# Optimization experiments

Hardware: AMD Instinct MI355X
Metric: run time of the kernel (lower is better)

The kernel has to match this reference:

```python
import jax, jax.numpy as jnp
import numpy as np

DIMS = [2048, 1024, 512, 256, 128, 64, 32, 16, 8, 4, 2]
IN_CH = [3, 8, 32, 64, 64, 64, 128, 256, 512, 512, 512]
FEAT = [8, 32, 64, 64, 64, 128, 256, 512, 512, 512, 1024]
B = 512
K = 16


def setup_inputs() -> dict:
    key = jax.random.key(0)
    keys = jax.random.split(key, 64)
    inp = {"x": jax.random.normal(keys[0], (B, 3, 2048), dtype=jnp.float32)}
    for i, d in enumerate(DIMS):
        inp[f"c{i}"] = jax.random.randint(keys[1 + i], (d,), 0, 3, dtype=jnp.int64)
    for i in range(11):
        cin, f = IN_CH[i], FEAT[i]
        inp[f"W{i+1}"] = jax.random.normal(keys[20 + 2 * i], (3 * f, cin), dtype=jnp.float32) / jnp.sqrt(jnp.float32(cin))
        inp[f"b{i+1}"] = jnp.zeros((3 * f,), dtype=jnp.float32)
    inp["Wfc"] = jax.random.normal(keys[60], (K, 1024), dtype=jnp.float32) / jnp.sqrt(jnp.float32(1024))
    inp["bfc"] = jnp.zeros((K,), dtype=jnp.float32)
    return inp


def _kdconv(x, W, b, sel, featdim, dim):
    # pointwise conv (kernel size 1) + relu: [B, in, dim] -> [B, 3*featdim, dim]
    y = jax.nn.relu(jnp.einsum('oi,bid->bod', W, x) + b[None, :, None])
    bsz = y.shape[0]
    # faithful to torch: view [B, featdim, 3*dim], then gather index d*3 + sel[d]
    y = y.reshape(bsz, featdim, 3 * dim)
    idx = sel + 3 * jnp.arange(dim, dtype=sel.dtype)
    y = jnp.take(y, idx, axis=2)                       # [B, featdim, dim]
    y = y.reshape(bsz, featdim, dim // 2, 2)
    return jnp.max(y, axis=-1)                          # [B, featdim, dim//2]


def reference(x, c0, c1, c2, c3, c4, c5, c6, c7, c8, c9, c10,
              W1, b1, W2, b2, W3, b3, W4, b4, W5, b5, W6, b6,
              W7, b7, W8, b8, W9, b9, W10, b10, W11, b11, Wfc, bfc):
    cs = [c0, c1, c2, c3, c4, c5, c6, c7, c8, c9, c10]
    Ws = [W1, W2, W3, W4, W5, W6, W7, W8, W9, W10, W11]
    bs = [b1, b2, b3, b4, b5, b6, b7, b8, b9, b10, b11]
    y = x
    for i in range(11):
        y = _kdconv(y, Ws[i], bs[i], cs[i], FEAT[i], DIMS[i])
    y = y.reshape(-1, 1024)
    logits = y @ Wfc.T + bfc
    return jax.nn.log_softmax(logits, axis=1)
```

## Files before the change

kernel.cpp:

```cpp
#include <hip/hip_runtime.h>
#include <cstdint>
#include <cmath>


typedef __attribute__((ext_vector_type(8))) short bhalf8;
typedef __attribute__((ext_vector_type(4))) float floatx4;

__device__ __forceinline__ unsigned short f2bf(float f) {
    uint32_t u = __float_as_uint(f);
    u += 0x7FFFu + ((u >> 16) & 1u);
    return (unsigned short)(u >> 16);
}
__device__ __forceinline__ float bf2f(unsigned short u) {
    return __uint_as_float(((uint32_t)u) << 16);
}

struct WPrep {
    const float* src[5];
    unsigned short* dst[5];
    int n4[5];
};

__global__ __launch_bounds__(256)
void wprep25_kernel(WPrep wp) {
    const int stride = gridDim.x * 256;
    const int g0 = blockIdx.x * 256 + threadIdx.x;
    #pragma unroll
    for (int l = 0; l < 4; ++l) {
        const float4* s = reinterpret_cast<const float4*>(wp.src[l]);
        uint2* d = reinterpret_cast<uint2*>(wp.dst[l]);
        for (int i = g0; i < wp.n4[l]; i += stride) {
            const float4 v = s[i];
            uint2 o;
            o.x = (uint32_t)f2bf(v.x) | ((uint32_t)f2bf(v.y) << 16);
            o.y = (uint32_t)f2bf(v.z) | ((uint32_t)f2bf(v.w) << 16);
            d[i] = o;
        }
    }
}


template<int RB>
__device__ __forceinline__ int swaddr(int row, int colbyte) {
    constexpr int SM = (RB / 16 >= 8) ? 7 : (RB / 16 - 1);
    return row * RB + (colbyte ^ ((row & SM) << 4));
}

template<int CIN>
__device__ __forceinline__ int wswz(int i) {
    constexpr int GPR = CIN / 8;
    constexpr int RB  = CIN * 2;
    const int row = i / GPR, c = i - row * GPR;
    return swaddr<RB>(row, c * 16);
}

template<int DIM, int CIN, int FEAT>
__device__ __forceinline__ void kdlayer(char* pool, int offIn, int offOut,
                                        int qpOff, int offW,
                                        const float* __restrict__ bg, int tid) {
    constexpr int NH  = CIN / 32;
    constexpr int MT  = DIM / 16;
    constexpr int NT  = FEAT / 16;
    constexpr int RBW = CIN * 2;
    constexpr int RBO = FEAT * 2;
    constexpr int WM  = (MT < 8) ? MT : 8;
    constexpr int WN  = 8 / WM;
    constexpr int MPW = MT / WM;
    constexpr int NPW = NT / WN;

    const unsigned short* qp = (const unsigned short*)(pool + qpOff);
    const int wv = tid >> 6, ln = tid & 63;
    const int g = ln >> 4, l15 = ln & 15;
    const int wm = wv % WM, wn = wv / WM;

    bhalf8 aC[MPW][NH];
    uint32_t qpk[MPW];
    #pragma unroll
    for (int i = 0; i < MPW; ++i) {
        const int mt = wm + i * WM;
        const int pa = qp[mt * 16 + l15] & 0xFFF;
        #pragma unroll
        for (int ks = 0; ks < NH; ++ks)
            aC[i][ks] = *(const bhalf8*)(pool + offIn +
                          swaddr<RBW>(pa, (ks * 32 + g * 8) * 2));
        const ushort4 qq = *(const ushort4*)(qp + mt * 16 + g * 4);
        qpk[i] = (uint32_t)(qq.x >> 12) | ((uint32_t)(qq.y >> 12) << 4)
               | ((uint32_t)(qq.z >> 12) << 8) | ((uint32_t)(qq.w >> 12) << 12);
    }

    #pragma unroll
    for (int ntj = 0; ntj < NPW; ++ntj) {
        const int nt = wn * NPW + ntj;
        const int f = nt * 16 + l15;
        bhalf8 bF[3][NH];
        #pragma unroll
        for (int q = 0; q < 3; ++q)
            #pragma unroll
            for (int ks = 0; ks < NH; ++ks)
                bF[q][ks] = *(const bhalf8*)(pool + offW +
                              swaddr<RBW>(3 * f + q, (ks * 32 + g * 8) * 2));
        const float bv0 = bg[3 * f + 0];
        const float bv1 = bg[3 * f + 1];
        const float bv2 = bg[3 * f + 2];
        #pragma unroll
        for (int i = 0; i < MPW; ++i) {
            floatx4 a0 = (floatx4){0.f,0.f,0.f,0.f};
            floatx4 a1 = (floatx4){0.f,0.f,0.f,0.f};
            floatx4 a2 = (floatx4){0.f,0.f,0.f,0.f};
            #pragma unroll
            for (int ks = 0; ks < NH; ++ks) {
                a0 = __builtin_amdgcn_mfma_f32_16x16x32_bf16(aC[i][ks], bF[0][ks], a0, 0, 0, 0);
                a1 = __builtin_amdgcn_mfma_f32_16x16x32_bf16(aC[i][ks], bF[1][ks], a1, 0, 0, 0);
                a2 = __builtin_amdgcn_mfma_f32_16x16x32_bf16(aC[i][ks], bF[2][ks], a2, 0, 0, 0);
            }
            const int mt = wm + i * WM;
            const int j0 = mt * 8 + g * 2;
            float v[4];
            #pragma unroll
            for (int r = 0; r < 4; ++r) {
                const int qi = (qpk[i] >> (4 * r)) & 0xF;
                const float pre = (qi == 0) ? a0[r] : (qi == 1 ? a1[r] : a2[r]);
                const float bq  = (qi == 0) ? bv0  : (qi == 1 ? bv1  : bv2);
                v[r] = pre + bq;
            }
            *(unsigned short*)(pool + offOut + swaddr<RBO>(j0,     f * 2)) =
                f2bf(fmaxf(fmaxf(v[0], v[1]), 0.f));
            *(unsigned short*)(pool + offOut + swaddr<RBO>(j0 + 1, f * 2)) =
                f2bf(fmaxf(fmaxf(v[2], v[3]), 0.f));
        }
    }
}

__global__ __launch_bounds__(512, 4)
void chain_kernel(const float* __restrict__ x,
                  const float* __restrict__ W0, const float* __restrict__ b0f,
                  const int* __restrict__ sel0,
                  const float* __restrict__ W1, const float* __restrict__ b1f,
                  const int* __restrict__ sel1,
                  unsigned short* __restrict__ outp,
                  const unsigned short* __restrict__ w2, const float* __restrict__ b2, const int* __restrict__ s2,
                  const unsigned short* __restrict__ w3, const float* __restrict__ b3, const int* __restrict__ s3,
                  const unsigned short* __restrict__ w4, const float* __restrict__ b4, const int* __restrict__ s4,
                  const unsigned short* __restrict__ w5, const float* __restrict__ b5, const int* __restrict__ s5,
                  WPrep wp, int nrows) {
    const int tid = threadIdx.x;

    if ((int)blockIdx.x >= nrows) {
        const int stride = (gridDim.x - nrows) * 512;
        const int g0 = (blockIdx.x - nrows) * 512 + tid;
        #pragma unroll
        for (int l = 0; l < 5; ++l) {
            const float4* s = reinterpret_cast<const float4*>(wp.src[l]);
            uint2* d = reinterpret_cast<uint2*>(wp.dst[l]);
            for (int i = g0; i < wp.n4[l]; i += stride) {
                const float4 v = s[i];
                uint2 o;
                o.x = (uint32_t)f2bf(v.x) | ((uint32_t)f2bf(v.y) << 16);
                o.y = (uint32_t)f2bf(v.z) | ((uint32_t)f2bf(v.w) << 16);
                d[i] = o;
            }
        }
        return;
    }

    __shared__ __align__(16) char pool[79872];
    const int b = blockIdx.x;

    bhalf8 w3r[3];
    #pragma unroll
    for (int u = 0; u < 3; ++u)
        w3r[u] = ((const bhalf8*)w3)[u * 512 + tid];
    bhalf8 w2r[2];
    w2r[0] = ((const bhalf8*)w2)[tid];
    if (tid < 256) w2r[1] = ((const bhalf8*)w2)[512 + tid];

    float* W0s = (float*)(pool + 47104);
    float* b0s = W0s + 72;
    float* W1s = b0s + 24;
    float* b1s = W1s + 768;
    if (tid < 24) {
        W0s[tid * 3 + 0] = W0[tid * 3 + 0];
        W0s[tid * 3 + 1] = W0[tid * 3 + 1];
        W0s[tid * 3 + 2] = W0[tid * 3 + 2];
        b0s[tid] = b0f[tid];
    }
    if (tid < 96) {
        #pragma unroll
        for (int k = 0; k < 8; ++k) W1s[tid * 8 + k] = W1[tid * 8 + k];
        b1s[tid] = b1f[tid];
    }
    {
        unsigned short* qp2 = (unsigned short*)(pool + 0);
        unsigned short* qp3 = (unsigned short*)(pool + 1024);
        unsigned short* qp4 = (unsigned short*)(pool + 1536);
        unsigned short* qp5 = (unsigned short*)(pool + 1792);
        { const int d = tid;
          const int e = 3 * d + s2[d];
          const int q = (e >= 512) + (e >= 1024);
          qp2[d] = (unsigned short)((q << 12) | (e - q * 512)); }
        if (tid < 256) { const int d = tid;
          const int e = 3 * d + s3[d];
          const int q = (e >= 256) + (e >= 512);
          qp3[d] = (unsigned short)((q << 12) | (e - q * 256)); }
        if (tid < 128) { const int d = tid;
          const int e = 3 * d + s4[d];
          const int q = (e >= 128) + (e >= 256);
          qp4[d] = (unsigned short)((q << 12) | (e - q * 128)); }
        if (tid < 64)  { const int d = tid;
          const int e = 3 * d + s5[d];
          const int q = (e >= 64) + (e >= 128);
          qp5[d] = (unsigned short)((q << 12) | (e - q * 64)); }
    }
    __syncthreads();

    {
        const int j1 = tid;
        const float* xb = x + (size_t)b * 3 * 2048;

        float cols[2][8];
        int q1v[2];
        #pragma unroll
        for (int pos1 = 0; pos1 < 2; ++pos1) {
            const int d1 = 2 * j1 + pos1;
            const int e1 = 3 * d1 + sel1[d1];
            const int q1 = (e1 >= 1024) + (e1 >= 2048);
            const int p1 = e1 - q1 * 1024;
            q1v[pos1] = q1;

            float xv[2][3]; int qq0[2];
            #pragma unroll
            for (int pos0 = 0; pos0 < 2; ++pos0) {
                const int d0 = 2 * p1 + pos0;
                const int e0 = 3 * d0 + sel0[d0];
                const int q0 = (e0 >= 2048) + (e0 >= 4096);
                const int p0 = e0 - q0 * 2048;
                qq0[pos0] = q0;
                xv[pos0][0] = xb[p0];
                xv[pos0][1] = xb[2048 + p0];
                xv[pos0][2] = xb[4096 + p0];
            }
            #pragma unroll
            for (int f = 0; f < 8; ++f) {
                const int r0 = 3 * f + qq0[0], r1 = 3 * f + qq0[1];
                const float v0 = b0s[r0] + W0s[r0*3+0]*xv[0][0] + W0s[r0*3+1]*xv[0][1] + W0s[r0*3+2]*xv[0][2];
                const float v1 = b0s[r1] + W0s[r1*3+0]*xv[1][0] + W0s[r1*3+1]*xv[1][1] + W0s[r1*3+2]*xv[1][2];
                cols[pos1][f] = fmaxf(fmaxf(v0, v1), 0.f);
            }
        }
        #pragma unroll
        for (int gi = 0; gi < 4; ++gi) {
            bhalf8 og;
            #pragma unroll
            for (int fk = 0; fk < 8; ++fk) {
                const int f = gi * 8 + fk;
                const int r0 = 3 * f + q1v[0], r1 = 3 * f + q1v[1];
                float v0 = b1s[r0], v1 = b1s[r1];
                #pragma unroll
                for (int k = 0; k < 8; ++k) {
                    v0 = fmaf(cols[0][k], W1s[r0*8+k], v0);
                    v1 = fmaf(cols[1][k], W1s[r1*8+k], v1);
                }
                og[fk] = (short)f2bf(fmaxf(fmaxf(v0, v1), 0.f));
            }
            *(bhalf8*)(pool + 2048 + swaddr<64>(j1, gi * 16)) = og;
        }
    }
    *(bhalf8*)(pool + 34816 + wswz<32>(tid)) = w2r[0];
    if (tid < 256)
        *(bhalf8*)(pool + 34816 + wswz<32>(512 + tid)) = w2r[1];
    __syncthreads();

    kdlayer<512, 32, 64>(pool, 2048, 47104, 0, 34816, b2, tid);
    __syncthreads();

    bhalf8 w4r[3];
    #pragma unroll
    for (int u = 0; u < 3; ++u)
        w4r[u] = ((const bhalf8*)w4)[u * 512 + tid];
    #pragma unroll
    for (int u = 0; u < 3; ++u)
        *(bhalf8*)(pool + 2048 + wswz<64>(u * 512 + tid)) = w3r[u];
    __syncthreads();

    kdlayer<256, 64, 64>(pool, 47104, 26624, 1024, 2048, b3, tid);
    __syncthreads();

    bhalf8 w5r[6];
    #pragma unroll
    for (int u = 0; u < 6; ++u)
        w5r[u] = ((const bhalf8*)w5)[u * 512 + tid];
    #pragma unroll
    for (int u = 0; u < 3; ++u)
        *(bhalf8*)(pool + 47104 + wswz<64>(u * 512 + tid)) = w4r[u];
    __syncthreads();

    kdlayer<128, 64, 64>(pool, 26624, 71680, 1536, 47104, b4, tid);
    __syncthreads();

    #pragma unroll
    for (int u = 0; u < 6; ++u)
        *(bhalf8*)(pool + 2048 + wswz<64>(u * 512 + tid)) = w5r[u];
    __syncthreads();

    kdlayer<64, 64, 128>(pool, 71680, 51200, 1792, 2048, b5, tid);
    __syncthreads();

    {
        char* dst = (char*)(outp + (size_t)b * 32 * 128);
        const int off = tid * 16;
        const bhalf8 v = *(const bhalf8*)(pool + 51200 +
                                          swaddr<256>(off >> 8, off & 255));
        *(bhalf8*)(dst + off) = v;
    }
}

template<int CIN, int BT>
__global__ __launch_bounds__(256)
void kdmfma_kernel(const unsigned short* __restrict__ act,
                   const unsigned short* __restrict__ Wq,
                   const float* __restrict__ bias,
                   const int*   __restrict__ sel,
                   unsigned short* __restrict__ out,
                   int feat, int dim, int nbt) {
    constexpr int KS  = (CIN >= 128) ? 128 : CIN;
    constexpr int NH  = KS / 32;
    constexpr int LDK = KS + 8;
    constexpr int TPA = 256 / BT;
    constexpr int EA  = KS / TPA;
    constexpr int NSA = EA / 8;
    constexpr int NSW = KS / 32;
    constexpr int MF  = 2;
    constexpr int NF  = (BT == 64) ? 2 : 1;
    __shared__ __align__(16) unsigned short Ab[BT][LDK];
    __shared__ __align__(16) unsigned short Wb[64][LDK];

    const int dimh = dim >> 1;
    const int bt = blockIdx.x % nbt;
    const int j  = blockIdx.x / nbt;
    const int f0 = blockIdx.y * 64;
    const int b0 = bt * BT;

    const int tid  = threadIdx.x;
    const int lane = tid & 63;
    const int wave = tid >> 6;

    const int srowA = tid / TPA;
    const int kgA   = (tid % TPA) * EA;
    const int srowW = tid >> 2;
    const int kgW   = (tid & 3) * (KS / 4);

    const int rowBase = (BT == 64) ? (wave & 1) * 32 : 0;
    const int colBase = (BT == 64) ? (wave >> 1) * 32 : wave * 16;

    floatx4 acc[2][MF][NF];
    #pragma unroll
    for (int pp = 0; pp < 2; ++pp)
        #pragma unroll
        for (int mi = 0; mi < MF; ++mi)
            #pragma unroll
            for (int ni = 0; ni < NF; ++ni)
                acc[pp][mi][ni] = (floatx4){0.f, 0.f, 0.f, 0.f};
    int qv[2];

    #pragma unroll
    for (int pp = 0; pp < 2; ++pp) {
        const int d = 2 * j + pp;
        const int s = sel[d];
        const int e = 3 * d + s;
        const int q = (e >= dim) + (e >= 2 * dim);
        const int p = e - q * dim;
        qv[pp] = q;

        const unsigned short* Ap = act + ((size_t)(b0 + srowA) * dim + p) * CIN + kgA;
        const unsigned short* Wp = Wq + ((size_t)(3 * (f0 + srowW) + q)) * CIN + kgW;

        bhalf8 pa[NSA], pw[NSW];
        #pragma unroll
        for (int u = 0; u < NSA; ++u)
            pa[u] = *reinterpret_cast<const bhalf8*>(Ap + u * 8);
        #pragma unroll
        for (int u = 0; u < NSW; ++u)
            pw[u] = *reinterpret_cast<const bhalf8*>(Wp + u * 8);

        for (int k0 = 0; k0 < CIN; k0 += KS) {
            __syncthreads();
            #pragma unroll
            for (int u = 0; u < NSA; ++u)
                *reinterpret_cast<bhalf8*>(&Ab[srowA][kgA + u * 8]) = pa[u];
            #pragma unroll
            for (int u = 0; u < NSW; ++u)
                *reinterpret_cast<bhalf8*>(&Wb[srowW][kgW + u * 8]) = pw[u];
            if (k0 + KS < CIN) {
                #pragma unroll
                for (int u = 0; u < NSA; ++u)
                    pa[u] = *reinterpret_cast<const bhalf8*>(Ap + k0 + KS + u * 8);
                #pragma unroll
                for (int u = 0; u < NSW; ++u)
                    pw[u] = *reinterpret_cast<const bhalf8*>(Wp + k0 + KS + u * 8);
            }
            __syncthreads();

            #pragma unroll
            for (int ks = 0; ks < NH; ++ks) {
                const int kk = ks * 32 + (lane >> 4) * 8;
                bhalf8 aF[MF], bF[NF];
                #pragma unroll
                for (int mi = 0; mi < MF; ++mi)
                    aF[mi] = *reinterpret_cast<const bhalf8*>(
                        &Ab[rowBase + mi * 16 + (lane & 15)][kk]);
                #pragma unroll
                for (int ni = 0; ni < NF; ++ni)
                    bF[ni] = *reinterpret_cast<const bhalf8*>(
                        &Wb[colBase + ni * 16 + (lane & 15)][kk]);
                #pragma unroll
                for (int mi = 0; mi < MF; ++mi)
                    #pragma unroll
                    for (int ni = 0; ni < NF; ++ni)
                        acc[pp][mi][ni] = __builtin_amdgcn_mfma_f32_16x16x32_bf16(
                            aF[mi], bF[ni], acc[pp][mi][ni], 0, 0, 0);
            }
        }
    }

    const int orow = (lane >> 4) << 2;
    const int ocol = lane & 15;
    #pragma unroll
    for (int mi = 0; mi < MF; ++mi)
        #pragma unroll
        for (int ni = 0; ni < NF; ++ni) {
            const int fc = f0 + colBase + ni * 16 + ocol;
            const float bv0 = bias[3 * fc + qv[0]];
            const float bv1 = bias[3 * fc + qv[1]];
            #pragma unroll
            for (int i = 0; i < 4; ++i) {
                const int br = b0 + rowBase + mi * 16 + orow + i;
                const float v = fmaxf(fmaxf(acc[0][mi][ni][i] + bv0,
                                            acc[1][mi][ni][i] + bv1), 0.f);
                out[((size_t)br * dimh + j) * feat + fc] = f2bf(v);
            }
        }
}

template<int CIN, int BT>
__global__ __launch_bounds__(256)
void kdmfma2_kernel(const unsigned short* __restrict__ act,
                    const unsigned short* __restrict__ Wq,
                    const float* __restrict__ bias,
                    const int*   __restrict__ sel,
                    unsigned short* __restrict__ out,
                    int feat, int dim, int nbt) {
    constexpr int KS  = 128;
    constexpr int NH  = KS / 32;
    constexpr int LDK = KS + 8;
    constexpr int TPA = 256 / BT;
    constexpr int EA  = KS / TPA;
    constexpr int NSA = EA / 8;
    constexpr int NSW = KS / 32;
    constexpr int MF  = 2;
    __shared__ __align__(16) unsigned short Ab[2][BT][LDK];
    __shared__ __align__(16) unsigned short Wb[2][64][LDK];

    const int dimh = dim >> 1;
    const int bt = blockIdx.x % nbt;
    const int j  = blockIdx.x / nbt;
    const int f0 = blockIdx.y * 64;
    const int b0 = bt * BT;

    const int tid  = threadIdx.x;
    const int lane = tid & 63;
    const int wave = tid >> 6;

    const int srowA = tid / TPA;
    const int kgA   = (tid % TPA) * EA;
    const int srowW = tid >> 2;
    const int kgW   = (tid & 3) * (KS / 4);
    const int colBase = wave * 16;

    int qv[2];
    const unsigned short* Ap[2];
    const unsigned short* Wp[2];
    #pragma unroll
    for (int pp = 0; pp < 2; ++pp) {
        const int d = 2 * j + pp;
        const int e = 3 * d + sel[d];
        const int q = (e >= dim) + (e >= 2 * dim);
        const int p = e - q * dim;
        qv[pp] = q;
        Ap[pp] = act + ((size_t)(b0 + srowA) * dim + p) * CIN + kgA;
        Wp[pp] = Wq + ((size_t)(3 * (f0 + srowW) + q)) * CIN + kgW;
    }

    floatx4 acc[2][MF];
    #pragma unroll
    for (int pp = 0; pp < 2; ++pp)
        #pragma unroll
        for (int mi = 0; mi < MF; ++mi)
            acc[pp][mi] = (floatx4){0.f, 0.f, 0.f, 0.f};

    bhalf8 pa[2][NSA], pw[2][NSW];
    #pragma unroll
    for (int pp = 0; pp < 2; ++pp) {
        #pragma unroll
        for (int u = 0; u < NSA; ++u)
            pa[pp][u] = *reinterpret_cast<const bhalf8*>(Ap[pp] + u * 8);
        #pragma unroll
        for (int u = 0; u < NSW; ++u)
            pw[pp][u] = *reinterpret_cast<const bhalf8*>(Wp[pp] + u * 8);
    }

    for (int k0 = 0; k0 < CIN; k0 += KS) {
        __syncthreads();
        #pragma unroll
        for (int pp = 0; pp < 2; ++pp) {
            #pragma unroll
            for (int u = 0; u < NSA; ++u)
                *reinterpret_cast<bhalf8*>(&Ab[pp][srowA][kgA + u * 8]) = pa[pp][u];
            #pragma unroll
            for (int u = 0; u < NSW; ++u)
                *reinterpret_cast<bhalf8*>(&Wb[pp][srowW][kgW + u * 8]) = pw[pp][u];
        }
        if (k0 + KS < CIN) {
            #pragma unroll
            for (int pp = 0; pp < 2; ++pp) {
                #pragma unroll
                for (int u = 0; u < NSA; ++u)
                    pa[pp][u] = *reinterpret_cast<const bhalf8*>(Ap[pp] + k0 + KS + u * 8);
                #pragma unroll
                for (int u = 0; u < NSW; ++u)
                    pw[pp][u] = *reinterpret_cast<const bhalf8*>(Wp[pp] + k0 + KS + u * 8);
            }
        }
        __syncthreads();

        #pragma unroll
        for (int ks = 0; ks < NH; ++ks) {
            const int kk = ks * 32 + (lane >> 4) * 8;
            bhalf8 aF[2][MF], bF[2];
            #pragma unroll
            for (int pp = 0; pp < 2; ++pp) {
                #pragma unroll
                for (int mi = 0; mi < MF; ++mi)
                    aF[pp][mi] = *reinterpret_cast<const bhalf8*>(
                        &Ab[pp][mi * 16 + (lane & 15)][kk]);
                bF[pp] = *reinterpret_cast<const bhalf8*>(
                        &Wb[pp][colBase + (lane & 15)][kk]);
            }
            #pragma unroll
            for (int pp = 0; pp < 2; ++pp)
                #pragma unroll
                for (int mi = 0; mi < MF; ++mi)
                    acc[pp][mi] = __builtin_amdgcn_mfma_f32_16x16x32_bf16(
                        aF[pp][mi], bF[pp], acc[pp][mi], 0, 0, 0);
        }
    }

    const int orow = (lane >> 4) << 2;
    const int ocol = lane & 15;
    #pragma unroll
    for (int mi = 0; mi < MF; ++mi) {
        const int fc = f0 + colBase + ocol;
        const float bv0 = bias[3 * fc + qv[0]];
        const float bv1 = bias[3 * fc + qv[1]];
        #pragma unroll
        for (int i = 0; i < 4; ++i) {
            const int br = b0 + mi * 16 + orow + i;
            const float v = fmaxf(fmaxf(acc[0][mi][i] + bv0,
                                        acc[1][mi][i] + bv1), 0.f);
            out[((size_t)br * dimh + j) * feat + fc] = f2bf(v);
        }
    }
}

__global__ __launch_bounds__(256)
void fc_lsm_kernel(const unsigned short* __restrict__ y,
                   const float* __restrict__ Wfc,
                   const float* __restrict__ bfc,
                   float* __restrict__ out) {
    const int b   = blockIdx.x;
    const int tid = threadIdx.x;
    __shared__ __align__(16) float ys[1024];
    __shared__ float lg[16];

    {
        const ushort4 v = reinterpret_cast<const ushort4*>(y + (size_t)b * 1024)[tid];
        ys[tid * 4 + 0] = bf2f(v.x);
        ys[tid * 4 + 1] = bf2f(v.y);
        ys[tid * 4 + 2] = bf2f(v.z);
        ys[tid * 4 + 3] = bf2f(v.w);
    }
    __syncthreads();

    const int l = tid >> 4, lane = tid & 15;
    const float4* w4 = reinterpret_cast<const float4*>(Wfc + (size_t)l * 1024);
    const float4* y4 = reinterpret_cast<const float4*>(ys);
    float p = 0.f;
    #pragma unroll
    for (int i = 0; i < 16; ++i) {
        const float4 a = y4[lane + 16 * i];
        const float4 w = w4[lane + 16 * i];
        p += a.x * w.x + a.y * w.y + a.z * w.z + a.w * w.w;
    }
    #pragma unroll
    for (int off = 8; off > 0; off >>= 1) p += __shfl_down(p, off, 16);
    if (lane == 0) lg[l] = p + bfc[l];
    __syncthreads();

    if (tid < 16) {
        float m = -1e30f;
        #pragma unroll
        for (int i = 0; i < 16; ++i) m = fmaxf(m, lg[i]);
        float s = 0.f;
        #pragma unroll
        for (int i = 0; i < 16; ++i) s += expf(lg[i] - m);
        out[b * 16 + tid] = lg[tid] - m - logf(s);
    }
}

extern "C" void kernel_launch(void* const* d_in, const int* in_sizes, int n_in,
                              void* d_out, int out_size, void* d_ws, size_t ws_size,
                              hipStream_t stream) {
    static const int LFEAT[11] = {8, 32, 64, 64, 64, 128, 256, 512, 512, 512, 1024};
    static const int LDIM[11]  = {2048, 1024, 512, 256, 128, 64, 32, 16, 8, 4, 2};
    static const int LCIN[11]  = {3, 8, 32, 64, 64, 64, 128, 256, 512, 512, 512};

    const float* x = (const float*)d_in[0];
    const int B = in_sizes[0] / (3 * 2048);

    const size_t slot = (size_t)B * 32 * 512;
    float* bufA = (float*)d_ws;
    float* bufB = bufA + slot;
    unsigned short* wq = (unsigned short*)(bufB + slot);

    const float* W[11]; const float* bi[11]; const int* sl[11];
    for (int i = 0; i < 11; ++i) {
        W[i]  = (const float*)d_in[12 + 2 * i];
        bi[i] = (const float*)d_in[13 + 2 * i];
        sl[i] = (const int*)d_in[1 + i];
    }

    unsigned short* wqp[11];
    {
        size_t off = 0;
        for (int i = 2; i <= 10; ++i) {
            wqp[i] = wq + off;
            off += (size_t)3 * LFEAT[i] * LCIN[i];
        }
    }

    unsigned short* actA = (unsigned short*)bufA;
    unsigned short* actB = (unsigned short*)bufB;

    {
        WPrep wp;
        for (int i = 2; i <= 5; ++i) {
            wp.src[i - 2] = W[i];
            wp.dst[i - 2] = wqp[i];
            wp.n4[i - 2]  = (3 * LFEAT[i] * LCIN[i]) / 4;
        }
        wp.src[4] = nullptr; wp.dst[4] = nullptr; wp.n4[4] = 0;
        wprep25_kernel<<<64, 256, 0, stream>>>(wp);
    }

    {
        WPrep wp;
        for (int i = 6; i <= 10; ++i) {
            wp.src[i - 6] = W[i];
            wp.dst[i - 6] = wqp[i];
            wp.n4[i - 6]  = (3 * LFEAT[i] * LCIN[i]) / 4;
        }
        chain_kernel<<<B + 256, 512, 0, stream>>>(
            x, W[0], bi[0], sl[0], W[1], bi[1], sl[1], actA,
            wqp[2], bi[2], sl[2], wqp[3], bi[3], sl[3],
            wqp[4], bi[4], sl[4], wqp[5], bi[5], sl[5],
            wp, B);
    }

    const int nbt64 = B / 64;
    const int nbt32 = B / 32;

    {   dim3 g((LDIM[6]/2) * nbt64, LFEAT[6]/64);
        kdmfma_kernel<128, 64><<<g, 256, 0, stream>>>(actA, wqp[6], bi[6], sl[6], actB, LFEAT[6], LDIM[6], nbt64); }
    {   dim3 g((LDIM[7]/2) * nbt64, LFEAT[7]/64);
        kdmfma_kernel<256, 64><<<g, 256, 0, stream>>>(actB, wqp[7], bi[7], sl[7], actA, LFEAT[7], LDIM[7], nbt64); }

    {   dim3 g((LDIM[8]/2) * nbt32, LFEAT[8]/64);
        kdmfma2_kernel<512, 32><<<g, 256, 0, stream>>>(actA, wqp[8], bi[8], sl[8], actB, LFEAT[8], LDIM[8], nbt32); }
    {   dim3 g((LDIM[9]/2) * nbt32, LFEAT[9]/64);
        kdmfma2_kernel<512, 32><<<g, 256, 0, stream>>>(actB, wqp[9], bi[9], sl[9], actA, LFEAT[9], LDIM[9], nbt32); }
    {   dim3 g((LDIM[10]/2) * nbt32, LFEAT[10]/64);
        kdmfma2_kernel<512, 32><<<g, 256, 0, stream>>>(actA, wqp[10], bi[10], sl[10], actB, LFEAT[10], LDIM[10], nbt32); }

    fc_lsm_kernel<<<B, 256, 0, stream>>>(actB, (const float*)d_in[34],
                                         (const float*)d_in[35], (float*)d_out);
}
```

Measured before the change: 82.31 us.

## Fuse layer 2-5 weight conversion into chain kernel and retile late MFMA layers

Drops the separate weight-prep kernel for layers 2-5; the chain kernel now reads fp32 weights and converts them to bf16 in registers before writing to shared memory. It also stages x and the layer-0 gather indices in LDS instead of reading them scattered from global memory. Layers 6-7 move from the older kdmfma kernel to kdmfma2 with 32-row batch tiles, and layers 9-10 use 16-row tiles to launch more blocks. The first-iteration barrier is skipped. In exchange the chain kernel holds more registers and reads twice the weight bytes, and the small-tile MFMA layers reuse less data per block.

Measured after the change: 86.69 us. 1.05x slower.

```diff
diff --git a/kernel.cpp b/kernel.cpp
--- a/kernel.cpp
+++ b/kernel.cpp
@@ -13,6 +13,14 @@
 }
 __device__ __forceinline__ float bf2f(unsigned short u) {
     return __uint_as_float(((uint32_t)u) << 16);
+}
+__device__ __forceinline__ bhalf8 cvt8(const float4 a, const float4 b) {
+    bhalf8 r;
+    r[0] = (short)f2bf(a.x); r[1] = (short)f2bf(a.y);
+    r[2] = (short)f2bf(a.z); r[3] = (short)f2bf(a.w);
+    r[4] = (short)f2bf(b.x); r[5] = (short)f2bf(b.y);
+    r[6] = (short)f2bf(b.z); r[7] = (short)f2bf(b.w);
+    return r;
 }
 
 struct WPrep {
@@ -20,25 +28,6 @@
     unsigned short* dst[5];
     int n4[5];
 };
-
-__global__ __launch_bounds__(256)
-void wprep25_kernel(WPrep wp) {
-    const int stride = gridDim.x * 256;
-    const int g0 = blockIdx.x * 256 + threadIdx.x;
-    #pragma unroll
-    for (int l = 0; l < 4; ++l) {
-        const float4* s = reinterpret_cast<const float4*>(wp.src[l]);
-        uint2* d = reinterpret_cast<uint2*>(wp.dst[l]);
-        for (int i = g0; i < wp.n4[l]; i += stride) {
-            const float4 v = s[i];
-            uint2 o;
-            o.x = (uint32_t)f2bf(v.x) | ((uint32_t)f2bf(v.y) << 16);
-            o.y = (uint32_t)f2bf(v.z) | ((uint32_t)f2bf(v.w) << 16);
-            d[i] = o;
-        }
-    }
-}
-
 
 template<int RB>
 __device__ __forceinline__ int swaddr(int row, int colbyte) {
@@ -138,10 +127,10 @@
                   const float* __restrict__ W1, const float* __restrict__ b1f,
                   const int* __restrict__ sel1,
                   unsigned short* __restrict__ outp,
-                  const unsigned short* __restrict__ w2, const float* __restrict__ b2, const int* __restrict__ s2,
-                  const unsigned short* __restrict__ w3, const float* __restrict__ b3, const int* __restrict__ s3,
-                  const unsigned short* __restrict__ w4, const float* __restrict__ b4, const int* __restrict__ s4,
-                  const unsigned short* __restrict__ w5, const float* __restrict__ b5, const int* __restrict__ s5,
+                  const float* __restrict__ w2f, const float* __restrict__ b2, const int* __restrict__ s2,
+                  const float* __restrict__ w3f, const float* __restrict__ b3, const int* __restrict__ s3,
+                  const float* __restrict__ w4f, const float* __restrict__ b4, const int* __restrict__ s4,
+                  const float* __restrict__ w5f, const float* __restrict__ b5, const int* __restrict__ s5,
                   WPrep wp, int nrows) {
     const int tid = threadIdx.x;
 
@@ -166,13 +155,21 @@
     __shared__ __align__(16) char pool[79872];
     const int b = blockIdx.x;
 
-    bhalf8 w3r[3];
-    #pragma unroll
-    for (int u = 0; u < 3; ++u)
-        w3r[u] = ((const bhalf8*)w3)[u * 512 + tid];
-    bhalf8 w2r[2];
-    w2r[0] = ((const bhalf8*)w2)[tid];
-    if (tid < 256) w2r[1] = ((const bhalf8*)w2)[512 + tid];
+    const float4* xg = (const float4*)(x + (size_t)b * 6144);
+    const float4 xr0 = xg[tid], xr1 = xg[512 + tid], xr2 = xg[1024 + tid];
+
+    const float4* w2g = (const float4*)w2f;
+    float4 w2a0 = w2g[2 * tid], w2a1 = w2g[2 * tid + 1];
+    float4 w2b0 = {0,0,0,0}, w2b1 = {0,0,0,0};
+    if (tid < 256) { w2b0 = w2g[2 * (512 + tid)]; w2b1 = w2g[2 * (512 + tid) + 1]; }
+
+    const float4* w3g = (const float4*)w3f;
+    float4 w3r[6];
+    #pragma unroll
+    for (int u = 0; u < 3; ++u) {
+        w3r[2 * u]     = w3g[2 * (u * 512 + tid)];
+        w3r[2 * u + 1] = w3g[2 * (u * 512 + tid) + 1];
+    }
 
     float* W0s = (float*)(pool + 47104);
     float* b0s = W0s + 72;
@@ -210,12 +207,25 @@
           const int e = 3 * d + s5[d];
           const int q = (e >= 64) + (e >= 128);
           qp5[d] = (unsigned short)((q << 12) | (e - q * 64)); }
+        unsigned short* qp0 = (unsigned short*)(pool + 75776);
+        #pragma unroll
+        for (int it = 0; it < 4; ++it) {
+            const int d = it * 512 + tid;
+            const int e = 3 * d + sel0[d];
+            const int q = (e >= 2048) + (e >= 4096);
+            qp0[d] = (unsigned short)((q << 12) | (e - q * 2048));
+        }
+    }
+    {
+        float4* xs4 = (float4*)(pool + 51200);
+        xs4[tid] = xr0; xs4[512 + tid] = xr1; xs4[1024 + tid] = xr2;
     }
     __syncthreads();
 
     {
         const int j1 = tid;
-        const float* xb = x + (size_t)b * 3 * 2048;
+        const float* xs = (const float*)(pool + 51200);
+        const unsigned short* qp0 = (const unsigned short*)(pool + 75776);
 
         float cols[2][8];
         int q1v[2];
@@ -230,14 +240,13 @@
             float xv[2][3]; int qq0[2];
             #pragma unroll
             for (int pos0 = 0; pos0 < 2; ++pos0) {
-                const int d0 = 2 * p1 + pos0;
-                const int e0 = 3 * d0 + sel0[d0];
-                const int q0 = (e0 >= 2048) + (e0 >= 4096);
-                const int p0 = e0 - q0 * 2048;
+                const int c0 = qp0[2 * p1 + pos0];
+                const int q0 = c0 >> 12;
+                const int p0 = c0 & 0xFFF;
                 qq0[pos0] = q0;
-                xv[pos0][0] = xb[p0];
-                xv[pos0][1] = xb[2048 + p0];
-                xv[pos0][2] = xb[4096 + p0];
+                xv[pos0][0] = xs[p0];
+                xv[pos0][1] = xs[2048 + p0];
+                xv[pos0][2] = xs[4096 + p0];
             }
             #pragma unroll
             for (int f = 0; f < 8; ++f) {
@@ -265,41 +274,47 @@
             *(bhalf8*)(pool + 2048 + swaddr<64>(j1, gi * 16)) = og;
         }
     }
-    *(bhalf8*)(pool + 34816 + wswz<32>(tid)) = w2r[0];
+    *(bhalf8*)(pool + 34816 + wswz<32>(tid)) = cvt8(w2a0, w2a1);
     if (tid < 256)
-        *(bhalf8*)(pool + 34816 + wswz<32>(512 + tid)) = w2r[1];
+        *(bhalf8*)(pool + 34816 + wswz<32>(512 + tid)) = cvt8(w2b0, w2b1);
     __syncthreads();
 
     kdlayer<512, 32, 64>(pool, 2048, 47104, 0, 34816, b2, tid);
     __syncthreads();
 
-    bhalf8 w4r[3];
+    const float4* w4g = (const float4*)w4f;
+    float4 w4r[6];
+    #pragma unroll
+    for (int u = 0; u < 3; ++u) {
+        w4r[2 * u]     = w4g[2 * (u * 512 + tid)];
+        w4r[2 * u + 1] = w4g[2 * (u * 512 + tid) + 1];
+    }
     #pragma unroll
     for (int u = 0; u < 3; ++u)
-        w4r[u] = ((const bhalf8*)w4)[u * 512 + tid];
+        *(bhalf8*)(pool + 2048 + wswz<64>(u * 512 + tid)) = cvt8(w3r[2*u], w3r[2*u+1]);
+    __syncthreads();
+
+    kdlayer<256, 64, 64>(pool, 47104, 26624, 1024, 2048, b3, tid);
+    __syncthreads();
+
+    const float4* w5g = (const float4*)w5f;
+    float4 w5r[12];
+    #pragma unroll
+    for (int u = 0; u < 6; ++u) {
+        w5r[2 * u]     = w5g[2 * (u * 512 + tid)];
+        w5r[2 * u + 1] = w5g[2 * (u * 512 + tid) + 1];
+    }
     #pragma unroll
     for (int u = 0; u < 3; ++u)
-        *(bhalf8*)(pool + 2048 + wswz<64>(u * 512 + tid)) = w3r[u];
-    __syncthreads();
-
-    kdlayer<256, 64, 64>(pool, 47104, 26624, 1024, 2048, b3, tid);
-    __syncthreads();
-
-    bhalf8 w5r[6];
+        *(bhalf8*)(pool + 47104 + wswz<64>(u * 512 + tid)) = cvt8(w4r[2*u], w4r[2*u+1]);
+    __syncthreads();
+
+    kdlayer<128, 64, 64>(pool, 26624, 71680, 1536, 47104, b4, tid);
+    __syncthreads();
+
     #pragma unroll
     for (int u = 0; u < 6; ++u)
-        w5r[u] = ((const bhalf8*)w5)[u * 512 + tid];
-    #pragma unroll
-    for (int u = 0; u < 3; ++u)
-        *(bhalf8*)(pool + 47104 + wswz<64>(u * 512 + tid)) = w4r[u];
-    __syncthreads();
-
-    kdlayer<128, 64, 64>(pool, 26624, 71680, 1536, 47104, b4, tid);
-    __syncthreads();
-
-    #pragma unroll
-    for (int u = 0; u < 6; ++u)
-        *(bhalf8*)(pool + 2048 + wswz<64>(u * 512 + tid)) = w5r[u];
+        *(bhalf8*)(pool + 2048 + wswz<64>(u * 512 + tid)) = cvt8(w5r[2*u], w5r[2*u+1]);
     __syncthreads();
 
     kdlayer<64, 64, 128>(pool, 71680, 51200, 1792, 2048, b5, tid);
@@ -312,133 +327,6 @@
                                           swaddr<256>(off >> 8, off & 255));
         *(bhalf8*)(dst + off) = v;
     }
-}
-
-template<int CIN, int BT>
-__global__ __launch_bounds__(256)
-void kdmfma_kernel(const unsigned short* __restrict__ act,
-                   const unsigned short* __restrict__ Wq,
-                   const float* __restrict__ bias,
-                   const int*   __restrict__ sel,
-                   unsigned short* __restrict__ out,
-                   int feat, int dim, int nbt) {
-    constexpr int KS  = (CIN >= 128) ? 128 : CIN;
-    constexpr int NH  = KS / 32;
-    constexpr int LDK = KS + 8;
-    constexpr int TPA = 256 / BT;
-    constexpr int EA  = KS / TPA;
-    constexpr int NSA = EA / 8;
-    constexpr int NSW = KS / 32;
-    constexpr int MF  = 2;
-    constexpr int NF  = (BT == 64) ? 2 : 1;
-    __shared__ __align__(16) unsigned short Ab[BT][LDK];
-    __shared__ __align__(16) unsigned short Wb[64][LDK];
-
-    const int dimh = dim >> 1;
-    const int bt = blockIdx.x % nbt;
-    const int j  = blockIdx.x / nbt;
-    const int f0 = blockIdx.y * 64;
-    const int b0 = bt * BT;
-
-    const int tid  = threadIdx.x;
-    const int lane = tid & 63;
-    const int wave = tid >> 6;
-
-    const int srowA = tid / TPA;
-    const int kgA   = (tid % TPA) * EA;
-    const int srowW = tid >> 2;
-    const int kgW   = (tid & 3) * (KS / 4);
-
-    const int rowBase = (BT == 64) ? (wave & 1) * 32 : 0;
-    const int colBase = (BT == 64) ? (wave >> 1) * 32 : wave * 16;
-
-    floatx4 acc[2][MF][NF];
-    #pragma unroll
-    for (int pp = 0; pp < 2; ++pp)
-        #pragma unroll
-        for (int mi = 0; mi < MF; ++mi)
-            #pragma unroll
-            for (int ni = 0; ni < NF; ++ni)
-                acc[pp][mi][ni] = (floatx4){0.f, 0.f, 0.f, 0.f};
-    int qv[2];
-
-    #pragma unroll
-    for (int pp = 0; pp < 2; ++pp) {
-        const int d = 2 * j + pp;
-        const int s = sel[d];
-        const int e = 3 * d + s;
-        const int q = (e >= dim) + (e >= 2 * dim);
-        const int p = e - q * dim;
-        qv[pp] = q;
-
-        const unsigned short* Ap = act + ((size_t)(b0 + srowA) * dim + p) * CIN + kgA;
-        const unsigned short* Wp = Wq + ((size_t)(3 * (f0 + srowW) + q)) * CIN + kgW;
-
-        bhalf8 pa[NSA], pw[NSW];
-        #pragma unroll
-        for (int u = 0; u < NSA; ++u)
-            pa[u] = *reinterpret_cast<const bhalf8*>(Ap + u * 8);
-        #pragma unroll
-        for (int u = 0; u < NSW; ++u)
-            pw[u] = *reinterpret_cast<const bhalf8*>(Wp + u * 8);
-
-        for (int k0 = 0; k0 < CIN; k0 += KS) {
-            __syncthreads();
-            #pragma unroll
-            for (int u = 0; u < NSA; ++u)
-                *reinterpret_cast<bhalf8*>(&Ab[srowA][kgA + u * 8]) = pa[u];
-            #pragma unroll
-            for (int u = 0; u < NSW; ++u)
-                *reinterpret_cast<bhalf8*>(&Wb[srowW][kgW + u * 8]) = pw[u];
-            if (k0 + KS < CIN) {
-                #pragma unroll
-                for (int u = 0; u < NSA; ++u)
-                    pa[u] = *reinterpret_cast<const bhalf8*>(Ap + k0 + KS + u * 8);
-                #pragma unroll
-                for (int u = 0; u < NSW; ++u)
-                    pw[u] = *reinterpret_cast<const bhalf8*>(Wp + k0 + KS + u * 8);
-            }
-            __syncthreads();
-
-            #pragma unroll
-            for (int ks = 0; ks < NH; ++ks) {
-                const int kk = ks * 32 + (lane >> 4) * 8;
-                bhalf8 aF[MF], bF[NF];
-                #pragma unroll
-                for (int mi = 0; mi < MF; ++mi)
-                    aF[mi] = *reinterpret_cast<const bhalf8*>(
-                        &Ab[rowBase + mi * 16 + (lane & 15)][kk]);
-                #pragma unroll
-                for (int ni = 0; ni < NF; ++ni)
-                    bF[ni] = *reinterpret_cast<const bhalf8*>(
-                        &Wb[colBase + ni * 16 + (lane & 15)][kk]);
-                #pragma unroll
-                for (int mi = 0; mi < MF; ++mi)
-                    #pragma unroll
-                    for (int ni = 0; ni < NF; ++ni)
-                        acc[pp][mi][ni] = __builtin_amdgcn_mfma_f32_16x16x32_bf16(
-                            aF[mi], bF[ni], acc[pp][mi][ni], 0, 0, 0);
-            }
-        }
-    }
-
-    const int orow = (lane >> 4) << 2;
-    const int ocol = lane & 15;
-    #pragma unroll
-    for (int mi = 0; mi < MF; ++mi)
-        #pragma unroll
-        for (int ni = 0; ni < NF; ++ni) {
-            const int fc = f0 + colBase + ni * 16 + ocol;
-            const float bv0 = bias[3 * fc + qv[0]];
-            const float bv1 = bias[3 * fc + qv[1]];
-            #pragma unroll
-            for (int i = 0; i < 4; ++i) {
-                const int br = b0 + rowBase + mi * 16 + orow + i;
-                const float v = fmaxf(fmaxf(acc[0][mi][ni][i] + bv0,
-                                            acc[1][mi][ni][i] + bv1), 0.f);
-                out[((size_t)br * dimh + j) * feat + fc] = f2bf(v);
-            }
-        }
 }
 
 template<int CIN, int BT>
@@ -456,7 +344,7 @@
     constexpr int EA  = KS / TPA;
     constexpr int NSA = EA / 8;
     constexpr int NSW = KS / 32;
-    constexpr int MF  = 2;
+    constexpr int MF  = BT / 16;
     __shared__ __align__(16) unsigned short Ab[2][BT][LDK];
     __shared__ __align__(16) unsigned short Wb[2][64][LDK];
 
@@ -509,7 +397,7 @@
     }
 
     for (int k0 = 0; k0 < CIN; k0 += KS) {
-        __syncthreads();
+        if (k0) __syncthreads();
         #pragma unroll
         for (int pp = 0; pp < 2; ++pp) {
             #pragma unroll
@@ -641,7 +529,7 @@
     unsigned short* wqp[11];
     {
         size_t off = 0;
-        for (int i = 2; i <= 10; ++i) {
+        for (int i = 6; i <= 10; ++i) {
             wqp[i] = wq + off;
             off += (size_t)3 * LFEAT[i] * LCIN[i];
         }
@@ -649,17 +537,6 @@
 
     unsigned short* actA = (unsigned short*)bufA;
     unsigned short* actB = (unsigned short*)bufB;
-
-    {
-        WPrep wp;
-        for (int i = 2; i <= 5; ++i) {
-            wp.src[i - 2] = W[i];
-            wp.dst[i - 2] = wqp[i];
-            wp.n4[i - 2]  = (3 * LFEAT[i] * LCIN[i]) / 4;
-        }
-        wp.src[4] = nullptr; wp.dst[4] = nullptr; wp.n4[4] = 0;
-        wprep25_kernel<<<64, 256, 0, stream>>>(wp);
-    }
 
     {
         WPrep wp;
@@ -670,25 +547,25 @@
         }
         chain_kernel<<<B + 256, 512, 0, stream>>>(
             x, W[0], bi[0], sl[0], W[1], bi[1], sl[1], actA,
-            wqp[2], bi[2], sl[2], wqp[3], bi[3], sl[3],
-            wqp[4], bi[4], sl[4], wqp[5], bi[5], sl[5],
+            W[2], bi[2], sl[2], W[3], bi[3], sl[3],
+            W[4], bi[4], sl[4], W[5], bi[5], sl[5],
             wp, B);
     }
 
-    const int nbt64 = B / 64;
     const int nbt32 = B / 32;
-
-    {   dim3 g((LDIM[6]/2) * nbt64, LFEAT[6]/64);
-        kdmfma_kernel<128, 64><<<g, 256, 0, stream>>>(actA, wqp[6], bi[6], sl[6], actB, LFEAT[6], LDIM[6], nbt64); }
-    {   dim3 g((LDIM[7]/2) * nbt64, LFEAT[7]/64);
-        kdmfma_kernel<256, 64><<<g, 256, 0, stream>>>(actB, wqp[7], bi[7], sl[7], actA, LFEAT[7], LDIM[7], nbt64); }
-
+    const int nbt16 = B / 16;
+
+    {   dim3 g((LDIM[6]/2) * nbt32, LFEAT[6]/64);
+        kdmfma2_kernel<128, 32><<<g, 256, 0, stream>>>(actA, wqp[6], bi[6], sl[6], actB, LFEAT[6], LDIM[6], nbt32); }
+    {   dim3 g((LDIM[7]/2) * nbt32, LFEAT[7]/64);
+        kdmfma2_kernel<256, 32><<<g, 256, 0, stream>>>(actB, wqp[7], bi[7], sl[7], actA, LFEAT[7], LDIM[7], nbt32); }
     {   dim3 g((LDIM[8]/2) * nbt32, LFEAT[8]/64);
         kdmfma2_kernel<512, 32><<<g, 256, 0, stream>>>(actA, wqp[8], bi[8], sl[8], actB, LFEAT[8], LDIM[8], nbt32); }
-    {   dim3 g((LDIM[9]/2) * nbt32, LFEAT[9]/64);
-        kdmfma2_kernel<512, 32><<<g, 256, 0, stream>>>(actB, wqp[9], bi[9], sl[9], actA, LFEAT[9], LDIM[9], nbt32); }
-    {   dim3 g((LDIM[10]/2) * nbt32, LFEAT[10]/64);
-        kdmfma2_kernel<512, 32><<<g, 256, 0, stream>>>(actA, wqp[10], bi[10], sl[10], actB, LFEAT[10], LDIM[10], nbt32); }
+
+    {   dim3 g((LDIM[9]/2) * nbt16, LFEAT[9]/64);
+        kdmfma2_kernel<512, 16><<<g, 256, 0, stream>>>(actB, wqp[9], bi[9], sl[9], actA, LFEAT[9], LDIM[9], nbt16); }
+    {   dim3 g((LDIM[10]/2) * nbt16, LFEAT[10]/64);
+        kdmfma2_kernel<512, 16><<<g, 256, 0, stream>>>(actA, wqp[10], bi[10], sl[10], actB, LFEAT[10], LDIM[10], nbt16); }
 
     fc_lsm_kernel<<<B, 256, 0, stream>>>(actB, (const float*)d_in[34],
                                          (const float*)d_in[35], (float*)d_out);
```
